# Kernel optimization log

Hardware: AMD Instinct MI355X
Metric: run time of the kernel (lower is better)

## Reference

```python
import jax, jax.numpy as jnp
import numpy as np

D = 512       # feature dim of X0 (Linear(512,...) in emb)
DQK = D // 8  # SAGAN-style reduced query/key dim
B = 256
S = 255       # structured features -> N = S + 1 tokens


def _lin(key, fan_in, fan_out):
    kw, kb = jax.random.split(key)
    s = 1.0 / np.sqrt(fan_in)
    W = jax.random.uniform(kw, (fan_in, fan_out), jnp.float32, -s, s)
    b = jax.random.uniform(kb, (fan_out,), jnp.float32, -s, s)
    return W, b


def setup_inputs() -> dict:
    key = jax.random.key(0)
    ks = jax.random.split(key, 9)
    X0 = jax.random.normal(ks[0], (B, D), jnp.float32)
    X_struc = jax.random.normal(ks[1], (B, S), jnp.float32)
    Wq, bq = _lin(ks[2], D, DQK)
    Wk, bk = _lin(ks[3], D, DQK)
    Wv, bv = _lin(ks[4], D, D)
    gamma = jnp.zeros((), jnp.float32) + 0.5  # nonzero so attention path contributes
    W1, b1 = _lin(ks[5], D, 1024)
    W2, b2 = _lin(ks[6], 1024, 512)
    W3, b3 = _lin(ks[7], 512, 128)
    return {"X0": X0, "X_struc": X_struc, "Wq": Wq, "bq": bq, "Wk": Wk, "bk": bk,
            "Wv": Wv, "bv": bv, "gamma": gamma, "W1": W1, "b1": b1,
            "W2": W2, "b2": b2, "W3": W3, "b3": b3}


def reference(X0, X_struc, Wq, bq, Wk, bk, Wv, bv, gamma, W1, b1, W2, b2, W3, b3):
    # Batched outer product replaces the per-sample torch.mm loop:
    # X1[b, s, d] = X_struc[b, s] * X0[b, d]
    X1 = X_struc[:, :, None] * X0[:, None, :]            # [B, S, D]
    X = jnp.concatenate([X0[:, None, :], X1], axis=1)    # [B, N, D], N = S+1
    # SAGAN-style self-attention (Self_Attention(out_planes=512))
    Q = X @ Wq + bq                                      # [B, N, DQK]
    K = X @ Wk + bk                                      # [B, N, DQK]
    V = X @ Wv + bv                                      # [B, N, D]
    A = jax.nn.softmax(jnp.einsum('bnc,bmc->bnm', Q, K), axis=-1)  # [B, N, N]
    Y = gamma * jnp.einsum('bnm,bmd->bnd', A, V) + X     # residual
    # emb MLP: 512 -> 1024 -> 512 -> 128, ReLU after each layer
    h = jax.nn.relu(Y @ W1 + b1)
    h = jax.nn.relu(h @ W2 + b2)
    out = jax.nn.relu(h @ W3 + b3)                       # [B, N, 128]
    return out
```

## Files before the change

kernel.cpp:

```cpp
#include <hip/hip_runtime.h>
#include <hip/hip_bf16.h>

typedef __attribute__((ext_vector_type(8))) short s16x8;
typedef __attribute__((ext_vector_type(16))) float f32x16;

__device__ __forceinline__ unsigned short f2bfu(float x) {
  __hip_bfloat16 b = __float2bfloat16(x);
  return *reinterpret_cast<unsigned short*>(&b);
}

__device__ __forceinline__ unsigned int cvtpk(float a, float b) {
  unsigned int r;
  asm("v_cvt_pk_bf16_f32 %0, %1, %2" : "=v"(r) : "v"(a), "v"(b));
  return r;
}

__global__ __launch_bounds__(256) void prep1_k(
    const float* __restrict__ W2, const float* __restrict__ W3,
    const float* __restrict__ W1,
    unsigned short* __restrict__ W2P, unsigned short* __restrict__ W3P,
    unsigned short* __restrict__ W1P,
    const float* __restrict__ X0, const float* __restrict__ Wv,
    const float* __restrict__ Wq, const float* __restrict__ Wk,
    float* __restrict__ V0ws, float* __restrict__ QKws) {
  __shared__ __align__(16) char smc[65664];
  const int tid = threadIdx.x;
  const int blk = blockIdx.x;

  if (blk < 64) {
    unsigned short* lt = (unsigned short*)smc;
    if (blk < 32) {
      const int kb = blk;
#pragma unroll
      for (int i = 0; i < 16; ++i) {
        const int e4 = i * 256 + tid;
        const int r = e4 >> 7, c4 = (e4 & 127) * 4;
        const float4 v = *(const float4*)(W2 + (size_t)(kb * 32 + r) * 512 + c4);
        lt[r * 514 + c4 + 0] = f2bfu(v.x);
        lt[r * 514 + c4 + 1] = f2bfu(v.y);
        lt[r * 514 + c4 + 2] = f2bfu(v.z);
        lt[r * 514 + c4 + 3] = f2bfu(v.w);
      }
      __syncthreads();
#pragma unroll
      for (int i = 0; i < 8; ++i) {
        const int c = i * 256 + tid;
        const int kgl = c >> 10, nb = (c >> 6) & 15, l = c & 63;
        const int col = nb * 32 + (l & 31);
        const int k0 = kgl * 16 + (l >> 5) * 8;
        s16x8 v;
#pragma unroll
        for (int j = 0; j < 8; ++j) v[j] = lt[(k0 + j) * 514 + col];
        *(s16x8*)(W2P + ((size_t)((kb * 2 + kgl) * 16 + nb) * 64 + l) * 8) = v;
      }
    } else if (blk < 48) {
      const int kb = blk - 32;
#pragma unroll
      for (int i = 0; i < 32; ++i) {
        const int e4 = i * 256 + tid;
        const int r = e4 >> 8, c4 = (e4 & 255) * 4;
        const float4 v = *(const float4*)(W1 + (size_t)(kb * 32 + r) * 1024 + c4);
        lt[r * 1026 + c4 + 0] = f2bfu(v.x);
        lt[r * 1026 + c4 + 1] = f2bfu(v.y);
        lt[r * 1026 + c4 + 2] = f2bfu(v.z);
        lt[r * 1026 + c4 + 3] = f2bfu(v.w);
      }
      __syncthreads();
#pragma unroll
      for (int i = 0; i < 16; ++i) {
        const int c = i * 256 + tid;
        const int kgl = c >> 11, nb = (c >> 6) & 31, l = c & 63;
        const int col = nb * 32 + (l & 31);
        const int k0 = kgl * 16 + (l >> 5) * 8;
        s16x8 v;
#pragma unroll
        for (int j = 0; j < 8; ++j) v[j] = lt[(k0 + j) * 1026 + col];
        *(s16x8*)(W1P + ((size_t)((kb * 2 + kgl) * 32 + nb) * 64 + l) * 8) = v;
      }
    } else {
      const int kb = blk - 48;
#pragma unroll
      for (int i = 0; i < 4; ++i) {
        const int e4 = i * 256 + tid;
        const int r = e4 >> 5, c4 = (e4 & 31) * 4;
        const float4 v = *(const float4*)(W3 + (size_t)(kb * 32 + r) * 128 + c4);
        lt[r * 130 + c4 + 0] = f2bfu(v.x);
        lt[r * 130 + c4 + 1] = f2bfu(v.y);
        lt[r * 130 + c4 + 2] = f2bfu(v.z);
        lt[r * 130 + c4 + 3] = f2bfu(v.w);
      }
      __syncthreads();
#pragma unroll
      for (int i = 0; i < 2; ++i) {
        const int c = i * 256 + tid;
        const int kgl = c >> 8, nb = (c >> 6) & 3, l = c & 63;
        const int col = nb * 32 + (l & 31);
        const int k0 = kgl * 16 + (l >> 5) * 8;
        s16x8 v;
#pragma unroll
        for (int j = 0; j < 8; ++j) v[j] = lt[(k0 + j) * 130 + col];
        *(s16x8*)(W3P + ((size_t)((kb * 2 + kgl) * 4 + nb) * 64 + l) * 8) = v;
      }
    }
    return;
  }
  float* x0f = (float*)smc;
  const int row = blk - 64;
  x0f[tid] = X0[(size_t)row * 512 + tid];
  x0f[tid + 256] = X0[(size_t)row * 512 + 256 + tid];
  __syncthreads();
  {
    float a0 = 0, a1 = 0, b0 = 0, b1 = 0;
#pragma unroll 8
    for (int k = 0; k < 512; k += 2) {
      const float xv0 = x0f[k], xv1 = x0f[k + 1];
      a0 = fmaf(xv0, Wv[(size_t)k * 512 + tid], a0);
      b0 = fmaf(xv1, Wv[(size_t)(k + 1) * 512 + tid], b0);
      a1 = fmaf(xv0, Wv[(size_t)k * 512 + tid + 256], a1);
      b1 = fmaf(xv1, Wv[(size_t)(k + 1) * 512 + tid + 256], b1);
    }
    V0ws[(size_t)row * 512 + tid] = a0 + b0;
    V0ws[(size_t)row * 512 + tid + 256] = a1 + b1;
  }
  if (tid < 128) {
    const float* W = (tid < 64) ? Wq : Wk;
    const int j = tid & 63;
    float a = 0, bpart = 0;
#pragma unroll 8
    for (int k = 0; k < 512; k += 2) {
      a = fmaf(x0f[k], W[(size_t)k * 64 + j], a);
      bpart = fmaf(x0f[k + 1], W[(size_t)(k + 1) * 64 + j], bpart);
    }
    QKws[(size_t)row * 128 + tid] = a + bpart;
  }
}

__global__ __launch_bounds__(256) void prep2_k(
    const float* __restrict__ Xs, const float* __restrict__ QKws,
    const float* __restrict__ bq, float* __restrict__ Wws,
    const float* __restrict__ V0ws, const float* __restrict__ X0,
    const float* __restrict__ bv, const float* __restrict__ W1,
    const unsigned short* __restrict__ W1P,
    const float* __restrict__ gp, const float* __restrict__ b1,
    float* __restrict__ Pws, float* __restrict__ Rws, float* __restrict__ Cws) {
  const int tid = threadIdx.x;
  if (blockIdx.x < 256) {
    const int b = blockIdx.x, t = tid;
    __shared__ float sv[256];
    __shared__ float scal[4];
    sv[t] = (t == 0) ? 1.0f : Xs[b * 255 + t - 1];
    __syncthreads();
    if (t == 0) {
      float al = 0, g2 = 0;
      for (int j = 0; j < 64; ++j) {
        al = fmaf(QKws[b * 128 + j], QKws[b * 128 + 64 + j], al);
        g2 = fmaf(bq[j], QKws[b * 128 + 64 + j], g2);
      }
      float mx = sv[0], mn = sv[0];
      for (int m2 = 1; m2 < 256; ++m2) { mx = fmaxf(mx, sv[m2]); mn = fminf(mn, sv[m2]); }
      scal[0] = al; scal[1] = g2; scal[2] = mx; scal[3] = mn;
    }
    __syncthreads();
    const float c = fmaf(scal[0], sv[tid], scal[1]);
    const float M = (c >= 0.f) ? c * scal[2] : c * scal[3];
    float Z = 0, Wm = 0;
    for (int m2 = 0; m2 < 256; ++m2) {
      const float e = __expf(fmaf(c, sv[m2], -M));
      Z += e;
      Wm = fmaf(sv[m2], e, Wm);
    }
    Wws[b * 256 + tid] = Wm / Z;
    return;
  }
  if (blockIdx.x < 260) {
    const int col = (blockIdx.x - 256) * 256 + tid;
    float a = 0;
    for (int d = 0; d < 512; ++d) a = fmaf(bv[d], W1[(size_t)d * 1024 + col], a);
    Cws[col] = fmaf(gp[0], a, b1[col]);
    return;
  }
  const int r = blockIdx.x - 260;
  const int pr = r >> 6;
  const int rem = r & 63;
  const int mb = rem >> 4, nb = rem & 15;
  const float* srcA = pr ? X0 : V0ws;
  float* dst = pr ? Rws : Pws;
  const int lane = tid & 63, w = tid >> 6;
  const int la31 = lane & 31, hi = lane >> 5;
  const int rowbase = mb * 64 + (w >> 1) * 32;
  const int nbW = nb * 2 + (w & 1);
  const float* ar = srcA + (size_t)(rowbase + la31) * 512 + hi * 8;
  const unsigned short* pBW = W1P + ((size_t)nbW * 64 + lane) * 8;

  f32x16 acc;
#pragma unroll
  for (int i = 0; i < 16; ++i) acc[i] = 0.f;

  float4 fa[2][2];
  s16x8 bst[2];
  fa[0][0] = *(const float4*)(ar);
  fa[0][1] = *(const float4*)(ar + 4);
  bst[0] = *(const s16x8*)(pBW);
  pBW += 16384;

#pragma unroll 2
  for (int kg = 0; kg < 32; ++kg) {
    const int par = kg & 1;
    if (kg < 31) {
      fa[par ^ 1][0] = *(const float4*)(ar + (kg + 1) * 16);
      fa[par ^ 1][1] = *(const float4*)(ar + (kg + 1) * 16 + 4);
      bst[par ^ 1] = *(const s16x8*)(pBW);
      pBW += 16384;
    }
    union { s16x8 v; unsigned int u[4]; } t;
    const float4 a0 = fa[par][0], a1 = fa[par][1];
    t.u[0] = cvtpk(a0.x, a0.y);
    t.u[1] = cvtpk(a0.z, a0.w);
    t.u[2] = cvtpk(a1.x, a1.y);
    t.u[3] = cvtpk(a1.z, a1.w);
    acc = __builtin_amdgcn_mfma_f32_32x32x16_bf16(t.v, bst[par], acc, 0, 0, 0);
  }
#pragma unroll
  for (int reg = 0; reg < 16; ++reg) {
    const int rowl = (reg & 3) + 8 * (reg >> 2) + 4 * hi;
    dst[(size_t)(rowbase + rowl) * 1024 + nbW * 32 + la31] = acc[reg];
  }
}

__global__ __launch_bounds__(1024, 4) void fused_k(
    const float* __restrict__ Xs, const float* __restrict__ gp,
    const unsigned short* __restrict__ W2P,
    const float* __restrict__ b2,
    const unsigned short* __restrict__ W3P,
    const float* __restrict__ b3,
    const float* __restrict__ Cws, const float* __restrict__ Wws,
    const float* __restrict__ Pws, const float* __restrict__ Rws,
    float* __restrict__ out)
{
  __shared__ __align__(16) unsigned char sm[131072];
  unsigned short* smU = (unsigned short*)sm;
  float* PRC = (float*)(sm + 65536);
  const int tid = threadIdx.x;
  const int lane = tid & 63, wid = tid >> 6;
  const int la31 = lane & 31, hi = lane >> 5;
  const int m0 = blockIdx.x * 128;
  const int b = blockIdx.x >> 1;
  const float g = gp[0];

  const int rg = tid & 127;
  const int ko = tid >> 7;
  const int tokg = (m0 & 255) + rg;
  const float gw = g * Wws[b * 256 + tokg];
  const float sr = (tokg == 0) ? 1.0f : Xs[b * 255 + tokg - 1];

#pragma unroll
  for (int i = 0; i < 3; ++i) {
    const int idx = i * 1024 + tid;
    float v;
    if (idx < 1024)      v = Pws[b * 1024 + idx];
    else if (idx < 2048) v = Rws[b * 1024 + (idx - 1024)];
    else                 v = Cws[idx - 2048];
    PRC[idx] = v;
  }

  auto gen = [&](int buf, int step) {
#pragma unroll
    for (int gsub = 0; gsub < 2; ++gsub) {
      const int s = gsub * 8 + ko;
      const int kb = step * 128 + s * 8;
      float e[8];
#pragma unroll
      for (int j = 0; j < 8; j += 4) {
        const float4 Pv = *(const float4*)(PRC + kb + j);
        const float4 Rv = *(const float4*)(PRC + 1024 + kb + j);
        const float4 Cv = *(const float4*)(PRC + 2048 + kb + j);
        e[j + 0] = fmaxf(fmaf(gw, Pv.x, fmaf(sr, Rv.x, Cv.x)), 0.f);
        e[j + 1] = fmaxf(fmaf(gw, Pv.y, fmaf(sr, Rv.y, Cv.y)), 0.f);
        e[j + 2] = fmaxf(fmaf(gw, Pv.z, fmaf(sr, Rv.z, Cv.z)), 0.f);
        e[j + 3] = fmaxf(fmaf(gw, Pv.w, fmaf(sr, Rv.w, Cv.w)), 0.f);
      }
      union { s16x8 v; unsigned int u[4]; } t0;
      t0.u[0] = cvtpk(e[0], e[1]);  t0.u[1] = cvtpk(e[2], e[3]);
      t0.u[2] = cvtpk(e[4], e[5]);  t0.u[3] = cvtpk(e[6], e[7]);
      *(s16x8*)(sm + buf * 32768 + (s * 128 + rg) * 16) = t0.v;
    }
  };

  f32x16 acc[4];
#pragma unroll
  for (int mf = 0; mf < 4; ++mf)
#pragma unroll
    for (int i = 0; i < 16; ++i) acc[mf][i] = 0.f;

  const unsigned short* pB = W2P + ((size_t)wid * 64 + lane) * 8;
  s16x8 bst[4];
#pragma unroll
  for (int d = 0; d < 3; ++d) {
    bst[d] = *(const s16x8*)(pB);
    pB += 8192;
  }

  __syncthreads();
  gen(0, 0);

  int kg = 0;
  for (int step = 0; step < 8; ++step) {
    __syncthreads();
    if (step < 7) gen((step + 1) & 1, step + 1);
    const int abase = (step & 1) * 32768;
#pragma unroll
    for (int kgl = 0; kgl < 8; ++kgl, ++kg) {
      bst[(kg + 3) & 3] = *(const s16x8*)(pB);
      pB += 8192;
      s16x8 af[4];
#pragma unroll
      for (int mf = 0; mf < 4; ++mf)
        af[mf] = *(const s16x8*)(sm + abase + ((kgl * 2 + hi) * 128 + mf * 32 + la31) * 16);
      const int cur = kg & 3;
      __builtin_amdgcn_s_setprio(1);
#pragma unroll
      for (int mf = 0; mf < 4; ++mf)
        acc[mf] = __builtin_amdgcn_mfma_f32_32x32x16_bf16(af[mf], bst[cur], acc[mf], 0, 0, 0);
      __builtin_amdgcn_s_setprio(0);
    }
  }
  __syncthreads();

  {
    const int col = wid * 32 + la31;
    const float bb = b2[col];
    const int sc = col >> 3, c7 = col & 7;
#pragma unroll
    for (int mf = 0; mf < 4; ++mf) {
#pragma unroll
      for (int reg = 0; reg < 16; ++reg) {
        const int row = mf * 32 + (reg & 3) + 8 * (reg >> 2) + 4 * hi;
        const int sp = (sc & 56) | ((sc ^ row) & 7);
        smU[row * 512 + sp * 8 + c7] = f2bfu(fmaxf(acc[mf][reg] + bb, 0.f));
      }
    }
  }
  __syncthreads();

  const int wr = wid >> 2, wc = wid & 3;
  f32x16 acc2;
#pragma unroll
  for (int i = 0; i < 16; ++i) acc2[i] = 0.f;

  const unsigned short* pW = W3P + ((size_t)wc * 64 + lane) * 8;
  s16x8 wst[4];
#pragma unroll
  for (int d = 0; d < 3; ++d) {
    wst[d] = *(const s16x8*)(pW);
    pW += 2048;
  }
#pragma unroll 4
  for (int kg2 = 0; kg2 < 32; ++kg2) {
    wst[(kg2 + 3) & 3] = *(const s16x8*)(pW);
    pW += 2048;
    const int s = kg2 * 2 + hi;
    const int row = wr * 32 + la31;
    const int sp = (s & 56) | ((s ^ row) & 7);
    const s16x8 afh = *(const s16x8*)(&sm[row * 1024 + (sp << 4)]);
    __builtin_amdgcn_s_setprio(1);
    acc2 = __builtin_amdgcn_mfma_f32_32x32x16_bf16(afh, wst[kg2 & 3], acc2, 0, 0, 0);
    __builtin_amdgcn_s_setprio(0);
  }

  {
    const int cB = wc * 32 + la31;
    const float b3v = b3[cB];
#pragma unroll
    for (int reg = 0; reg < 16; ++reg) {
      const int row = m0 + wr * 32 + (reg & 3) + 8 * (reg >> 2) + 4 * hi;
      out[(size_t)row * 128 + cB] = fmaxf(acc2[reg] + b3v, 0.f);
    }
  }
}

extern "C" void kernel_launch(void* const* d_in, const int* in_sizes, int n_in,
                              void* d_out, int out_size, void* d_ws, size_t ws_size,
                              hipStream_t stream) {
  const float* X0 = (const float*)d_in[0];
  const float* Xs = (const float*)d_in[1];
  const float* Wq = (const float*)d_in[2];
  const float* bq = (const float*)d_in[3];
  const float* Wk = (const float*)d_in[4];
  const float* bk = (const float*)d_in[5];
  const float* Wv = (const float*)d_in[6];
  const float* bv = (const float*)d_in[7];
  const float* gp = (const float*)d_in[8];
  const float* W1 = (const float*)d_in[9];
  const float* b1 = (const float*)d_in[10];
  const float* W2 = (const float*)d_in[11];
  const float* b2 = (const float*)d_in[12];
  const float* W3 = (const float*)d_in[13];
  const float* b3 = (const float*)d_in[14];

  char* ws = (char*)d_ws;
  float* Cws = (float*)(ws);
  float* Wws = (float*)(ws + 4096);
  float* Pws = (float*)(ws + 266240);
  float* Rws = (float*)(ws + 1314816);
  unsigned short* W2P = (unsigned short*)(ws + 2363392);
  unsigned short* W3P = (unsigned short*)(ws + 3411968);
  float* V0ws = (float*)(ws + 3543040);
  float* QKws = (float*)(ws + 4067328);
  unsigned short* W1P = (unsigned short*)(ws + 4198400);
  float* out = (float*)d_out;

  hipLaunchKernelGGL(prep1_k, dim3(320), dim3(256), 0, stream,
                     W2, W3, W1, W2P, W3P, W1P, X0, Wv, Wq, Wk, V0ws, QKws);
  hipLaunchKernelGGL(prep2_k, dim3(388), dim3(256), 0, stream,
                     Xs, QKws, bq, Wws, V0ws, X0, bv, W1, W1P, gp, b1, Pws, Rws, Cws);
  hipLaunchKernelGGL(fused_k, dim3(512), dim3(1024), 0, stream,
                     Xs, gp, W2P, b2, W3P, b3, Cws, Wws, Pws, Rws, out);
}
```

Measured before the change: 125.4 us.

## Restructure fused MLP kernel to 64-row tiles with register-generated activations

The fused layer-2/3 kernel moves from 128-token blocks of 1024 threads to 64-token blocks of 512 threads, doubling the grid. The layer-2 GEMM is transposed: the weight tile becomes the MFMA A operand, and each lane builds the layer-1 ReLU activation fragment directly in registers from the shared P/R/C vectors. This removes the double-buffered LDS staging of activations and the per-step barriers. Shared memory drops to about 76KB, which should allow more blocks per CU. The cost is that each W2 fragment is reused across fewer tokens, so weight loads per token double and the lane-level activation arithmetic is repeated across waves.

Result: slower. 151.2 us (+20.6%).

```diff
diff --git a/kernel.cpp b/kernel.cpp
--- a/kernel.cpp
+++ b/kernel.cpp
@@ -227,7 +227,7 @@
   }
 }
 
-__global__ __launch_bounds__(1024, 4) void fused_k(
+__global__ __launch_bounds__(512, 4) void fused_k(
     const float* __restrict__ Xs, const float* __restrict__ gp,
     const unsigned short* __restrict__ W2P,
     const float* __restrict__ b2,
@@ -237,25 +237,25 @@
     const float* __restrict__ Pws, const float* __restrict__ Rws,
     float* __restrict__ out)
 {
-  __shared__ __align__(16) unsigned char sm[131072];
+  __shared__ __align__(16) unsigned char sm[77824];
   unsigned short* smU = (unsigned short*)sm;
   float* PRC = (float*)(sm + 65536);
   const int tid = threadIdx.x;
   const int lane = tid & 63, wid = tid >> 6;
   const int la31 = lane & 31, hi = lane >> 5;
-  const int m0 = blockIdx.x * 128;
-  const int b = blockIdx.x >> 1;
+  const int tm = wid >> 2, tn = wid & 3;
+  const int m0 = blockIdx.x * 64;
+  const int b = blockIdx.x >> 2;
   const float g = gp[0];
 
-  const int rg = tid & 127;
-  const int ko = tid >> 7;
-  const int tokg = (m0 & 255) + rg;
-  const float gw = g * Wws[b * 256 + tokg];
-  const float sr = (tokg == 0) ? 1.0f : Xs[b * 255 + tokg - 1];
-
-#pragma unroll
-  for (int i = 0; i < 3; ++i) {
-    const int idx = i * 1024 + tid;
+  const int tokL = tm * 32 + la31;
+  const int tok = (m0 & 255) + tokL;
+  const float gw = g * Wws[b * 256 + tok];
+  const float sr = (tok == 0) ? 1.0f : Xs[b * 255 + tok - 1];
+
+#pragma unroll
+  for (int i = 0; i < 6; ++i) {
+    const int idx = i * 512 + tid;
     float v;
     if (idx < 1024)      v = Pws[b * 1024 + idx];
     else if (idx < 2048) v = Rws[b * 1024 + (idx - 1024)];
@@ -263,81 +263,67 @@
     PRC[idx] = v;
   }
 
-  auto gen = [&](int buf, int step) {
-#pragma unroll
-    for (int gsub = 0; gsub < 2; ++gsub) {
-      const int s = gsub * 8 + ko;
-      const int kb = step * 128 + s * 8;
-      float e[8];
-#pragma unroll
-      for (int j = 0; j < 8; j += 4) {
-        const float4 Pv = *(const float4*)(PRC + kb + j);
-        const float4 Rv = *(const float4*)(PRC + 1024 + kb + j);
-        const float4 Cv = *(const float4*)(PRC + 2048 + kb + j);
-        e[j + 0] = fmaxf(fmaf(gw, Pv.x, fmaf(sr, Rv.x, Cv.x)), 0.f);
-        e[j + 1] = fmaxf(fmaf(gw, Pv.y, fmaf(sr, Rv.y, Cv.y)), 0.f);
-        e[j + 2] = fmaxf(fmaf(gw, Pv.z, fmaf(sr, Rv.z, Cv.z)), 0.f);
-        e[j + 3] = fmaxf(fmaf(gw, Pv.w, fmaf(sr, Rv.w, Cv.w)), 0.f);
-      }
-      union { s16x8 v; unsigned int u[4]; } t0;
-      t0.u[0] = cvtpk(e[0], e[1]);  t0.u[1] = cvtpk(e[2], e[3]);
-      t0.u[2] = cvtpk(e[4], e[5]);  t0.u[3] = cvtpk(e[6], e[7]);
-      *(s16x8*)(sm + buf * 32768 + (s * 128 + rg) * 16) = t0.v;
-    }
-  };
-
   f32x16 acc[4];
 #pragma unroll
-  for (int mf = 0; mf < 4; ++mf)
-#pragma unroll
-    for (int i = 0; i < 16; ++i) acc[mf][i] = 0.f;
-
-  const unsigned short* pB = W2P + ((size_t)wid * 64 + lane) * 8;
-  s16x8 bst[4];
-#pragma unroll
-  for (int d = 0; d < 3; ++d) {
-    bst[d] = *(const s16x8*)(pB);
-    pB += 8192;
+  for (int nf = 0; nf < 4; ++nf)
+#pragma unroll
+    for (int i = 0; i < 16; ++i) acc[nf][i] = 0.f;
+
+  const unsigned short* pA = W2P + ((size_t)(tn * 4) * 64 + lane) * 8;
+  s16x8 ast[2][4];
+#pragma unroll
+  for (int d = 0; d < 2; ++d) {
+#pragma unroll
+    for (int nf = 0; nf < 4; ++nf)
+      ast[d][nf] = *(const s16x8*)(pA + nf * 512);
+    pA += 8192;
   }
 
   __syncthreads();
-  gen(0, 0);
-
-  int kg = 0;
-  for (int step = 0; step < 8; ++step) {
-    __syncthreads();
-    if (step < 7) gen((step + 1) & 1, step + 1);
-    const int abase = (step & 1) * 32768;
-#pragma unroll
-    for (int kgl = 0; kgl < 8; ++kgl, ++kg) {
-      bst[(kg + 3) & 3] = *(const s16x8*)(pB);
-      pB += 8192;
-      s16x8 af[4];
-#pragma unroll
-      for (int mf = 0; mf < 4; ++mf)
-        af[mf] = *(const s16x8*)(sm + abase + ((kgl * 2 + hi) * 128 + mf * 32 + la31) * 16);
-      const int cur = kg & 3;
-      __builtin_amdgcn_s_setprio(1);
-#pragma unroll
-      for (int mf = 0; mf < 4; ++mf)
-        acc[mf] = __builtin_amdgcn_mfma_f32_32x32x16_bf16(af[mf], bst[cur], acc[mf], 0, 0, 0);
-      __builtin_amdgcn_s_setprio(0);
-    }
-  }
-  __syncthreads();
-
-  {
-    const int col = wid * 32 + la31;
-    const float bb = b2[col];
-    const int sc = col >> 3, c7 = col & 7;
-#pragma unroll
-    for (int mf = 0; mf < 4; ++mf) {
-#pragma unroll
-      for (int reg = 0; reg < 16; ++reg) {
-        const int row = mf * 32 + (reg & 3) + 8 * (reg >> 2) + 4 * hi;
-        const int sp = (sc & 56) | ((sc ^ row) & 7);
-        smU[row * 512 + sp * 8 + c7] = f2bfu(fmaxf(acc[mf][reg] + bb, 0.f));
-      }
+
+#pragma unroll 2
+  for (int kg = 0; kg < 64; ++kg) {
+    const int cur = kg & 1;
+    const int kb = kg * 16 + hi * 8;
+    const float4 P0 = *(const float4*)(PRC + kb);
+    const float4 P1 = *(const float4*)(PRC + kb + 4);
+    const float4 R0 = *(const float4*)(PRC + 1024 + kb);
+    const float4 R1 = *(const float4*)(PRC + 1024 + kb + 4);
+    const float4 C0 = *(const float4*)(PRC + 2048 + kb);
+    const float4 C1 = *(const float4*)(PRC + 2048 + kb + 4);
+    const float e0 = fmaxf(fmaf(gw, P0.x, fmaf(sr, R0.x, C0.x)), 0.f);
+    const float e1 = fmaxf(fmaf(gw, P0.y, fmaf(sr, R0.y, C0.y)), 0.f);
+    const float e2 = fmaxf(fmaf(gw, P0.z, fmaf(sr, R0.z, C0.z)), 0.f);
+    const float e3 = fmaxf(fmaf(gw, P0.w, fmaf(sr, R0.w, C0.w)), 0.f);
+    const float e4 = fmaxf(fmaf(gw, P1.x, fmaf(sr, R1.x, C1.x)), 0.f);
+    const float e5 = fmaxf(fmaf(gw, P1.y, fmaf(sr, R1.y, C1.y)), 0.f);
+    const float e6 = fmaxf(fmaf(gw, P1.z, fmaf(sr, R1.z, C1.z)), 0.f);
+    const float e7 = fmaxf(fmaf(gw, P1.w, fmaf(sr, R1.w, C1.w)), 0.f);
+    union { s16x8 v; unsigned int u[4]; } bf;
+    bf.u[0] = cvtpk(e0, e1);
+    bf.u[1] = cvtpk(e2, e3);
+    bf.u[2] = cvtpk(e4, e5);
+    bf.u[3] = cvtpk(e6, e7);
+    __builtin_amdgcn_s_setprio(1);
+#pragma unroll
+    for (int nf = 0; nf < 4; ++nf)
+      acc[nf] = __builtin_amdgcn_mfma_f32_32x32x16_bf16(ast[cur][nf], bf.v, acc[nf], 0, 0, 0);
+    __builtin_amdgcn_s_setprio(0);
+#pragma unroll
+    for (int nf = 0; nf < 4; ++nf)
+      ast[cur][nf] = *(const s16x8*)(pA + nf * 512);
+    pA += 8192;
+  }
+
+#pragma unroll
+  for (int nf = 0; nf < 4; ++nf) {
+#pragma unroll
+    for (int reg = 0; reg < 16; ++reg) {
+      const int outcol = tn * 128 + nf * 32 + (reg & 3) + 8 * (reg >> 2) + 4 * hi;
+      const float v = fmaxf(acc[nf][reg] + b2[outcol], 0.f);
+      const int o = outcol >> 3;
+      const int sp = (o & 56) | ((o ^ tokL) & 7);
+      smU[tokL * 512 + sp * 8 + (outcol & 7)] = f2bfu(v);
     }
   }
   __syncthreads();
@@ -413,6 +399,6 @@
                      W2, W3, W1, W2P, W3P, W1P, X0, Wv, Wq, Wk, V0ws, QKws);
   hipLaunchKernelGGL(prep2_k, dim3(388), dim3(256), 0, stream,
                      Xs, QKws, bq, Wws, V0ws, X0, bv, W1, W1P, gp, b1, Pws, Rws, Cws);
-  hipLaunchKernelGGL(fused_k, dim3(512), dim3(1024), 0, stream,
+  hipLaunchKernelGGL(fused_k, dim3(1024), dim3(512), 0, stream,
                      Xs, gp, W2P, b2, W3P, b3, Cws, Wws, Pws, Rws, out);
 }
```
